# Kernel optimization log

Hardware: AMD Instinct MI355X
Metric: run time of the kernel (lower is better)

Reference implementation:

```python
import jax, jax.numpy as jnp
import numpy as np
import math

D_MODEL = 512
N_HEADS = 8
D_HEAD = D_MODEL // N_HEADS
TEMP = math.sqrt(D_HEAD)


def setup_inputs() -> dict:
    key = jax.random.key(0)
    k1, k2, k3, k4, k5, k6 = jax.random.split(key, 6)
    B, L = 4, 2048
    q = jax.random.normal(k1, (B, L, D_MODEL), dtype=jnp.float32)
    # bool mask, True -> zero out post-softmax attention (matches torch.where branch)
    mask = jax.random.bernoulli(k2, 0.1, (B, L, L))
    in_weight = jax.random.normal(k3, (3 * D_MODEL, D_MODEL), dtype=jnp.float32) * 0.02
    in_bias = jax.random.normal(k4, (3 * D_MODEL,), dtype=jnp.float32) * 0.02
    out_w = jax.random.normal(k5, (D_MODEL, D_MODEL), dtype=jnp.float32) * 0.02
    out_b = jax.random.normal(k6, (D_MODEL,), dtype=jnp.float32) * 0.02
    return {"q": q, "mask": mask, "in_weight": in_weight, "in_bias": in_bias,
            "out_w": out_w, "out_b": out_b}


def reference(q, mask, in_weight, in_bias, out_w, out_b):
    B, L, D = q.shape
    # per-head weight slicing exactly as the torch reshape: (H, E, 3, D)
    W = in_weight.reshape(N_HEADS, D_HEAD, 3, D)
    Bv = in_bias.reshape(N_HEADS, D_HEAD, 3)
    qw, kw, vw = W[:, :, 0, :], W[:, :, 1, :], W[:, :, 2, :]  # (H, E, D)
    qb, kb, vb = Bv[:, :, 0], Bv[:, :, 1], Bv[:, :, 2]        # (H, E)
    # self-attention: k = q, v = q (forward defaults)
    Q = jnp.einsum('bld,hed->bhle', q, qw) + qb[None, :, None, :]
    K = jnp.einsum('bld,hed->bhle', q, kw) + kb[None, :, None, :]
    V = jnp.einsum('bld,hed->bhle', q, vw) + vb[None, :, None, :]
    atn = jax.nn.softmax(jnp.einsum('bhqe,bhke->bhqk', Q, K) / TEMP, axis=-1)
    # post-softmax bool masking (faithful to the original non-standard order)
    atn = jnp.where(mask[:, None, :, :], jnp.zeros((), atn.dtype), atn)
    # QUIRK of source: attention() returns V (not atn @ V); heads = concat of V
    heads = V.transpose(0, 2, 1, 3).reshape(B, L, D)  # (B, L, D_MODEL)
    outputs = heads @ out_w.T + out_b
    masks = atn.sum(axis=1)  # sum over heads -> (B, Lq, Lk)
    return outputs, masks
```

## Files before the change

### kernel.cpp

```cpp
#include <hip/hip_runtime.h>

typedef unsigned short u16;
typedef unsigned int u32;
typedef __bf16 bf16x8 __attribute__((ext_vector_type(8)));
typedef float f32x4 __attribute__((ext_vector_type(4)));

#define B_SZ 4
#define L_SZ 2048
#define D_SZ 512
#define H_SZ 8
#define E_SZ 64

#define Q_SCALE 0.18033688011112042f

#define WS_FLAG   0
#define WS_WPACK  1024
#define WS_BPACK  (WS_WPACK + 1572864)
#define WS_WOUT   (WS_BPACK + 6144)
#define WS_QBF    (WS_WOUT + 524288)
#define WS_Q      (WS_QBF + 8388608)
#define WS_K      (WS_Q + 8388608)
#define WS_V      (WS_K + 8388608)
#define WS_STATS  (WS_V + 8388608)

static __device__ __forceinline__ u16 f2bf(float f) {
  unsigned int u = __float_as_uint(f);
  u += 0x7FFFu + ((u >> 16) & 1u);
  return (u16)(u >> 16);
}

static __device__ __forceinline__ float fexp2(float x) {
  return __builtin_amdgcn_exp2f(x);
}

union FragU { bf16x8 v; uint4 u4; unsigned long long ul[2]; };

static __device__ __forceinline__ int gperm(int d) {
  int t = d & 31;
  return (d & ~31) | ((t & 12) << 1) | ((t & 16) >> 2) | (t & 3);
}

static __device__ __forceinline__ bf16x8 qfrag(const u16* __restrict__ Qp,
                                               int row, int half, int lg) {
  FragU f;
  f.u4 = *reinterpret_cast<const uint4*>(
      (const char*)Qp + (size_t)row * 128 + (half << 6) + (lg << 4));
  return f.v;
}

static __device__ __forceinline__ void gload_lds16(const void* g, void* l) {
  __builtin_amdgcn_global_load_lds(
      (const __attribute__((address_space(1))) void*)g,
      (__attribute__((address_space(3))) void*)l, 16, 0, 0);
}

template<int NT, int NCHUNK>
static __device__ __forceinline__ void stage_ktile(const u16* __restrict__ Kh, int kb0,
                                                   char* tile, int tid) {
  int wbase = (tid & ~63) * 16;
#pragma unroll
  for (int i = 0; i < NCHUNK / NT; i++) {
    int cl = tid + i * NT;
    int r = cl >> 3, c = cl & 7;
    const char* g = (const char*)Kh + (size_t)(kb0 + r) * 128 + ((c ^ (r & 7)) << 4);
    gload_lds16(g, tile + wbase + i * NT * 16);
  }
}

static __device__ __forceinline__ bf16x8 lds_frag(const char* tile, int c, int half,
                                                  int lr, int lg) {
  int r = c * 16 + lr;
  int off = ((half << 6) | (lg << 4)) ^ ((r & 7) << 4);
  FragU f;
  f.u4 = *reinterpret_cast<const uint4*>(tile + r * 128 + off);
  return f.v;
}

__global__ __launch_bounds__(256) void kdetect(const unsigned int* __restrict__ w,
                                               int* __restrict__ flag) {
  int fB = 0, fF = 0;
  for (int i = blockIdx.x * blockDim.x + threadIdx.x; i < 262144;
       i += gridDim.x * blockDim.x) {
    unsigned int v = w[i];
    if (v == 0x3F800000u) fF = 1;
    else if (v > 1u) fB = 1;
  }
  if (__any(fB)) { if ((threadIdx.x & 63) == 0) atomicOr(&flag[0], 1); }
  if (__any(fF)) { if ((threadIdx.x & 63) == 0) atomicOr(&flag[1], 1); }
}

__global__ __launch_bounds__(256) void kcast(const float* __restrict__ q,
                                             u16* __restrict__ qbf) {
  int i = blockIdx.x * blockDim.x + threadIdx.x;
  int row = i >> 6, c = i & 63;
  int g = c >> 2, lg = c & 3;
  const float* src = q + (size_t)row * 512 + g * 32 + lg * 4;
  float4 v0 = *reinterpret_cast<const float4*>(src);
  float4 v1 = *reinterpret_cast<const float4*>(src + 16);
  u32 w0 = f2bf(v0.x) | ((u32)f2bf(v0.y) << 16);
  u32 w1 = f2bf(v0.z) | ((u32)f2bf(v0.w) << 16);
  u32 w2 = f2bf(v1.x) | ((u32)f2bf(v1.y) << 16);
  u32 w3 = f2bf(v1.z) | ((u32)f2bf(v1.w) << 16);
  uint4 out = {w0, w1, w2, w3};
  *reinterpret_cast<uint4*>(qbf + (size_t)row * 512 + c * 8) = out;
}

__global__ __launch_bounds__(256) void kpack(const float* __restrict__ w_in,
                                             const float* __restrict__ b_in,
                                             const float* __restrict__ w_out,
                                             u16* __restrict__ Wpack, float* __restrict__ bpack,
                                             u16* __restrict__ Wout) {
  const int T0 = 1536 * 512;
  const int T1 = T0 + 512 * 512;
  const int T2 = T1 + 1536;
  for (int i = blockIdx.x * blockDim.x + threadIdx.x; i < T2; i += gridDim.x * blockDim.x) {
    if (i < T0) {
      int n = i >> 9, d = i & 511;
      int sel = n >> 9, idx = n & 511;
      int h = idx >> 6, e = idx & 63;
      int row = h * 192 + e * 3 + sel;
      float v = w_in[row * 512 + d];
      if (sel == 0) v *= Q_SCALE;
      Wpack[(size_t)n * 512 + gperm(d)] = f2bf(v);
    } else if (i < T1) {
      int j = i - T0;
      int n = j >> 9, d = j & 511;
      Wout[(size_t)n * 512 + gperm(d)] = f2bf(w_out[j]);
    } else {
      int n = i - T1;
      int sel = n >> 9, idx = n & 511;
      int h = idx >> 6, e = idx & 63;
      int row = h * 192 + e * 3 + sel;
      float v = b_in[row];
      if (sel == 0) v *= Q_SCALE;
      bpack[n] = v;
    }
  }
}

static __device__ __forceinline__ void stage_tile(const u16* __restrict__ A,
                                                  const u16* __restrict__ Bw,
                                                  int m0, int n0, int t,
                                                  char* tA, char* tB, int tid) {
  int w64 = tid & ~63;
#pragma unroll
  for (int i = 0; i < 4; i++) {
    int cl = tid + i * 256;
    int r = cl >> 3, c = cl & 7;
    size_t gofs = (size_t)r * 1024 + t * 128 + ((c ^ (r & 7)) << 4);
    gload_lds16((const char*)A + (size_t)m0 * 1024 + gofs, tA + (i * 256 + w64) * 16);
    gload_lds16((const char*)Bw + (size_t)n0 * 1024 + gofs, tB + (i * 256 + w64) * 16);
  }
}

template<int MODE>
__global__ __launch_bounds__(256) void kgemm(const u16* __restrict__ A,
                                             const u16* __restrict__ Bw,
                                             const float* __restrict__ bias,
                                             u16* __restrict__ Qb, u16* __restrict__ Kb,
                                             u16* __restrict__ Vb, float* __restrict__ outp) {
  __shared__ __align__(128) char tA[2][16384], tB[2][16384];
  int tid = threadIdx.x;
  int w = tid >> 6, lane = tid & 63;
  int lr = lane & 15, lg = lane >> 4;
  int m0 = blockIdx.x * 128, n0 = blockIdx.y * 128;
  int wr = w >> 1, wc = w & 1;

  f32x4 acc[4][4] = {};

  stage_tile(A, Bw, m0, n0, 0, tA[0], tB[0], tid);
  __syncthreads();
#pragma unroll 1
  for (int t = 0; t < 8; t++) {
    if (t < 7) stage_tile(A, Bw, m0, n0, t + 1, tA[(t + 1) & 1], tB[(t + 1) & 1], tid);
    const char* mA = tA[t & 1] + wr * 64 * 128;
    const char* mB = tB[t & 1] + wc * 64 * 128;
#pragma unroll
    for (int gg = 0; gg < 2; gg++) {
      bf16x8 af[4], bf_[4];
#pragma unroll
      for (int i = 0; i < 4; i++) af[i] = lds_frag(mA, i, gg, lr, lg);
#pragma unroll
      for (int j = 0; j < 4; j++) bf_[j] = lds_frag(mB, j, gg, lr, lg);
#pragma unroll
      for (int i = 0; i < 4; i++)
#pragma unroll
        for (int j = 0; j < 4; j++)
          acc[i][j] = __builtin_amdgcn_mfma_f32_16x16x32_bf16(af[i], bf_[j], acc[i][j], 0, 0, 0);
    }
    __syncthreads();
  }

#pragma unroll
  for (int j = 0; j < 4; j++) {
    int col = n0 + wc * 64 + j * 16 + lr;
    float bb = bias[col];
#pragma unroll
    for (int i = 0; i < 4; i++) {
#pragma unroll
      for (int jj = 0; jj < 4; jj++) {
        int row = m0 + wr * 64 + i * 16 + lg * 4 + jj;
        float val = acc[i][j][jj] + bb;
        if (MODE == 1) {
          outp[(size_t)row * 512 + col] = val;
        } else {
          u16 bv = f2bf(val);
          int b = row >> 11, l = row & 2047;
          if (col < 512) {
            int h = col >> 6, e = col & 63;
            Qb[((((size_t)(b * 8 + h)) << 11) + l) * 64 + gperm(e)] = bv;
          } else if (col < 1024) {
            int c2 = col - 512, h = c2 >> 6, e = c2 & 63;
            Kb[((((size_t)(b * 8 + h)) << 11) + l) * 64 + gperm(e)] = bv;
          } else {
            Vb[(size_t)row * 512 + gperm(col - 1024)] = bv;
          }
        }
      }
    }
  }
}

__global__ __launch_bounds__(256, 4) void kstats(const u16* __restrict__ Qb,
                                                 const u16* __restrict__ Kb,
                                                 float* __restrict__ stats) {
  __shared__ __align__(128) char tile[2][8192];
  int bh = blockIdx.x;
  int tid = threadIdx.x;
  int w = tid >> 6, lane = tid & 63;
  int lr = lane & 15, lg = lane >> 4;
  int q0 = blockIdx.y * 64 + w * 16;
  const u16* Qp = Qb + (size_t)bh * L_SZ * E_SZ;
  const u16* Kp = Kb + (size_t)bh * L_SZ * E_SZ;

  bf16x8 bq0 = qfrag(Qp, q0 + lr, 0, lg);
  bf16x8 bq1 = qfrag(Qp, q0 + lr, 1, lg);
  float s0 = 0.0f;

  stage_ktile<256, 512>(Kp, 0, tile[0], tid);
  __syncthreads();
#pragma unroll 1
  for (int t = 0; t < 32; t++) {
    if (t + 1 < 32) stage_ktile<256, 512>(Kp, (t + 1) * 64, tile[(t + 1) & 1], tid);
    const char* tl = tile[t & 1];
#pragma unroll
    for (int c = 0; c < 4; c++) {
      bf16x8 a0 = lds_frag(tl, c, 0, lr, lg);
      bf16x8 a1 = lds_frag(tl, c, 1, lr, lg);
      f32x4 d = {0.f, 0.f, 0.f, 0.f};
      d = __builtin_amdgcn_mfma_f32_16x16x32_bf16(a0, bq0, d, 0, 0, 0);
      d = __builtin_amdgcn_mfma_f32_16x16x32_bf16(a1, bq1, d, 0, 0, 0);
      s0 += fexp2(d[0]) + fexp2(d[1]) + fexp2(d[2]) + fexp2(d[3]);
    }
    __syncthreads();
  }
  s0 += __shfl_xor(s0, 16);
  s0 += __shfl_xor(s0, 32);
  if (lane < 16) stats[(size_t)bh * L_SZ + q0 + lr] = 1.0f / s0;
}

#define KM_PACKMASK(BITS, QOFS)                                                  \
  {                                                                              \
    size_t moff = mb + (size_t)(q0 + (QOFS) + lr) * L_SZ + kb0;                  \
    if (mode == 0) {                                                             \
      _Pragma("unroll")                                                          \
      for (int c = 0; c < 2; c++) {                                              \
        int4 mi = *reinterpret_cast<const int4*>((const int*)mask + moff + c * 16 + lg * 4); \
        BITS |= (mi.x ? 1u : 0u) << (c * 4);                                     \
        BITS |= (mi.y ? 1u : 0u) << (c * 4 + 1);                                 \
        BITS |= (mi.z ? 1u : 0u) << (c * 4 + 2);                                 \
        BITS |= (mi.w ? 1u : 0u) << (c * 4 + 3);                                 \
      }                                                                          \
    } else if (mode == 1) {                                                      \
      _Pragma("unroll")                                                          \
      for (int c = 0; c < 2; c++) {                                              \
        u32 mw = *reinterpret_cast<const u32*>((const unsigned char*)mask + moff + c * 16 + lg * 4); \
        BITS |= ((mw & 0x000000FFu) ? 1u : 0u) << (c * 4);                       \
        BITS |= ((mw & 0x0000FF00u) ? 1u : 0u) << (c * 4 + 1);                   \
        BITS |= ((mw & 0x00FF0000u) ? 1u : 0u) << (c * 4 + 2);                   \
        BITS |= ((mw & 0xFF000000u) ? 1u : 0u) << (c * 4 + 3);                   \
      }                                                                          \
    } else {                                                                     \
      _Pragma("unroll")                                                          \
      for (int c = 0; c < 2; c++) {                                              \
        float4 mf = *reinterpret_cast<const float4*>((const float*)mask + moff + c * 16 + lg * 4); \
        BITS |= ((mf.x != 0.f) ? 1u : 0u) << (c * 4);                            \
        BITS |= ((mf.y != 0.f) ? 1u : 0u) << (c * 4 + 1);                        \
        BITS |= ((mf.z != 0.f) ? 1u : 0u) << (c * 4 + 2);                        \
        BITS |= ((mf.w != 0.f) ? 1u : 0u) << (c * 4 + 3);                        \
      }                                                                          \
    }                                                                            \
  }

__global__ __launch_bounds__(256, 4) void kmasks(const u16* __restrict__ Qb,
                                                 const u16* __restrict__ Kb,
                                                 const float* __restrict__ stats,
                                                 const void* __restrict__ mask,
                                                 const int* __restrict__ flag,
                                                 float* __restrict__ outp) {
  __shared__ __align__(128) char tile[32768];
  int b = blockIdx.z;
  int tid = threadIdx.x;
  int lane = tid & 63;
  int lr = lane & 15, lg = lane >> 4;
  int w = tid >> 6;
  int q0 = blockIdx.y * 64 + w * 16;
  int kb0 = blockIdx.x * 32;
  int mode = flag[0] ? 1 : (flag[1] ? 2 : 0);
  const size_t LE = (size_t)L_SZ * E_SZ;
  size_t mb = (size_t)b * L_SZ * L_SZ;

  {
    int wbase = (tid & ~63) * 16;
#pragma unroll
    for (int i = 0; i < 8; i++) {
      int r = tid >> 3, cc = tid & 7;
      const char* g = (const char*)(Kb + (size_t)(b * 8 + i) * LE)
                    + (size_t)(kb0 + r) * 128 + ((cc ^ (r & 7)) << 4);
      gload_lds16(g, tile + (i * 256 + (tid & ~63)) * 16 + (wbase - (tid & ~63) * 16));
    }
  }

  bf16x8 qh0[8], qh1[8];
  float rr[8];
#pragma unroll
  for (int h = 0; h < 8; h++) {
    const u16* Qp = Qb + (size_t)(b * 8 + h) * LE;
    qh0[h] = qfrag(Qp, q0 + lr, 0, lg);
    qh1[h] = qfrag(Qp, q0 + lr, 1, lg);
    rr[h] = stats[(size_t)(b * 8 + h) * L_SZ + q0 + lr];
  }

  u32 bits0 = 0;
  KM_PACKMASK(bits0, 0)

  __syncthreads();

  f32x4 P0 = {0.f, 0.f, 0.f, 0.f}, P1 = {0.f, 0.f, 0.f, 0.f};
#pragma unroll
  for (int h = 0; h < 8; h++) {
    const char* th = tile + h * 4096;
    {
      bf16x8 a0 = lds_frag(th, 0, 0, lr, lg);
      bf16x8 a1 = lds_frag(th, 0, 1, lr, lg);
      f32x4 d = {0.f, 0.f, 0.f, 0.f};
      d = __builtin_amdgcn_mfma_f32_16x16x32_bf16(a0, qh0[h], d, 0, 0, 0);
      d = __builtin_amdgcn_mfma_f32_16x16x32_bf16(a1, qh1[h], d, 0, 0, 0);
#pragma unroll
      for (int j = 0; j < 4; j++) P0[j] += fexp2(d[j]) * rr[h];
    }
    {
      bf16x8 a0 = lds_frag(th, 1, 0, lr, lg);
      bf16x8 a1 = lds_frag(th, 1, 1, lr, lg);
      f32x4 d = {0.f, 0.f, 0.f, 0.f};
      d = __builtin_amdgcn_mfma_f32_16x16x32_bf16(a0, qh0[h], d, 0, 0, 0);
      d = __builtin_amdgcn_mfma_f32_16x16x32_bf16(a1, qh1[h], d, 0, 0, 0);
#pragma unroll
      for (int j = 0; j < 4; j++) P1[j] += fexp2(d[j]) * rr[h];
    }
  }

  float* mrow = outp + (size_t)B_SZ * L_SZ * D_SZ + mb
              + (size_t)(q0 + lr) * L_SZ + kb0;
  {
    f32x4 v = P0;
    if ((bits0 >> 0) & 1u) v[0] = 0.f;
    if ((bits0 >> 1) & 1u) v[1] = 0.f;
    if ((bits0 >> 2) & 1u) v[2] = 0.f;
    if ((bits0 >> 3) & 1u) v[3] = 0.f;
    *reinterpret_cast<f32x4*>(mrow + lg * 4) = v;
  }
  {
    f32x4 v = P1;
    if ((bits0 >> 4) & 1u) v[0] = 0.f;
    if ((bits0 >> 5) & 1u) v[1] = 0.f;
    if ((bits0 >> 6) & 1u) v[2] = 0.f;
    if ((bits0 >> 7) & 1u) v[3] = 0.f;
    *reinterpret_cast<f32x4*>(mrow + 16 + lg * 4) = v;
  }
}

extern "C" void kernel_launch(void* const* d_in, const int* in_sizes, int n_in,
                              void* d_out, int out_size, void* d_ws, size_t ws_size,
                              hipStream_t stream) {
  (void)in_sizes; (void)n_in; (void)out_size; (void)ws_size;
  const float* q     = (const float*)d_in[0];
  const void*  mask  = d_in[1];
  const float* w_in  = (const float*)d_in[2];
  const float* b_in  = (const float*)d_in[3];
  const float* w_out = (const float*)d_in[4];
  const float* b_out = (const float*)d_in[5];
  float* outp = (float*)d_out;
  char* ws = (char*)d_ws;

  int*    flag  = (int*)(ws + WS_FLAG);
  u16*    Wpack = (u16*)(ws + WS_WPACK);
  float*  bpack = (float*)(ws + WS_BPACK);
  u16*    Wout  = (u16*)(ws + WS_WOUT);
  u16*    qbf   = (u16*)(ws + WS_QBF);
  u16*    Qb    = (u16*)(ws + WS_Q);
  u16*    Kb    = (u16*)(ws + WS_K);
  u16*    Vb    = (u16*)(ws + WS_V);
  float*  stats = (float*)(ws + WS_STATS);

  hipMemsetAsync(flag, 0, 16, stream);
  hipLaunchKernelGGL(kdetect, dim3(256), dim3(256), 0, stream, (const unsigned int*)mask, flag);
  hipLaunchKernelGGL(kcast, dim3(2048), dim3(256), 0, stream, q, qbf);
  hipLaunchKernelGGL(kpack, dim3(2048), dim3(256), 0, stream, w_in, b_in, w_out,
                     Wpack, bpack, Wout);
  hipLaunchKernelGGL((kgemm<0>), dim3(64, 12), dim3(256), 0, stream,
                     qbf, Wpack, bpack, Qb, Kb, Vb, (float*)nullptr);
  hipLaunchKernelGGL((kgemm<1>), dim3(64, 4), dim3(256), 0, stream,
                     Vb, Wout, b_out, (u16*)nullptr, (u16*)nullptr, (u16*)nullptr, outp);
  hipLaunchKernelGGL(kstats, dim3(32, 32), dim3(256), 0, stream, Qb, Kb, stats);
  hipLaunchKernelGGL(kmasks, dim3(64, 32, 4), dim3(256), 0, stream, Qb, Kb, stats, mask, flag, outp);
}
```

Measured before the change: 168.0 us.

## Enlarge kmasks tiles to reuse staged K across more query rows

The mask kernel now uses 512-thread blocks that stage a 64-key K tile for all 8 heads (64KB of LDS) once, then loop over 512 query rows in four 128-row chunks. Before, each block staged a 32-key tile and handled only 64 query rows. The goal is to cut redundant global K traffic and LDS staging per output element. In exchange, Q fragments and stats are now reloaded per head inside the loop, and the grid shrinks to 512 blocks with large LDS use, which lowers occupancy and latency hiding.

```diff
diff --git a/kernel.cpp b/kernel.cpp
--- a/kernel.cpp
+++ b/kernel.cpp
@@ -259,53 +259,20 @@
   if (lane < 16) stats[(size_t)bh * L_SZ + q0 + lr] = 1.0f / s0;
 }
 
-#define KM_PACKMASK(BITS, QOFS)                                                  \
-  {                                                                              \
-    size_t moff = mb + (size_t)(q0 + (QOFS) + lr) * L_SZ + kb0;                  \
-    if (mode == 0) {                                                             \
-      _Pragma("unroll")                                                          \
-      for (int c = 0; c < 2; c++) {                                              \
-        int4 mi = *reinterpret_cast<const int4*>((const int*)mask + moff + c * 16 + lg * 4); \
-        BITS |= (mi.x ? 1u : 0u) << (c * 4);                                     \
-        BITS |= (mi.y ? 1u : 0u) << (c * 4 + 1);                                 \
-        BITS |= (mi.z ? 1u : 0u) << (c * 4 + 2);                                 \
-        BITS |= (mi.w ? 1u : 0u) << (c * 4 + 3);                                 \
-      }                                                                          \
-    } else if (mode == 1) {                                                      \
-      _Pragma("unroll")                                                          \
-      for (int c = 0; c < 2; c++) {                                              \
-        u32 mw = *reinterpret_cast<const u32*>((const unsigned char*)mask + moff + c * 16 + lg * 4); \
-        BITS |= ((mw & 0x000000FFu) ? 1u : 0u) << (c * 4);                       \
-        BITS |= ((mw & 0x0000FF00u) ? 1u : 0u) << (c * 4 + 1);                   \
-        BITS |= ((mw & 0x00FF0000u) ? 1u : 0u) << (c * 4 + 2);                   \
-        BITS |= ((mw & 0xFF000000u) ? 1u : 0u) << (c * 4 + 3);                   \
-      }                                                                          \
-    } else {                                                                     \
-      _Pragma("unroll")                                                          \
-      for (int c = 0; c < 2; c++) {                                              \
-        float4 mf = *reinterpret_cast<const float4*>((const float*)mask + moff + c * 16 + lg * 4); \
-        BITS |= ((mf.x != 0.f) ? 1u : 0u) << (c * 4);                            \
-        BITS |= ((mf.y != 0.f) ? 1u : 0u) << (c * 4 + 1);                        \
-        BITS |= ((mf.z != 0.f) ? 1u : 0u) << (c * 4 + 2);                        \
-        BITS |= ((mf.w != 0.f) ? 1u : 0u) << (c * 4 + 3);                        \
-      }                                                                          \
-    }                                                                            \
-  }
-
-__global__ __launch_bounds__(256, 4) void kmasks(const u16* __restrict__ Qb,
+__global__ __launch_bounds__(512, 4) void kmasks(const u16* __restrict__ Qb,
                                                  const u16* __restrict__ Kb,
                                                  const float* __restrict__ stats,
                                                  const void* __restrict__ mask,
                                                  const int* __restrict__ flag,
                                                  float* __restrict__ outp) {
-  __shared__ __align__(128) char tile[32768];
+  __shared__ __align__(128) char tile[65536];
   int b = blockIdx.z;
   int tid = threadIdx.x;
   int lane = tid & 63;
   int lr = lane & 15, lg = lane >> 4;
   int w = tid >> 6;
-  int q0 = blockIdx.y * 64 + w * 16;
-  int kb0 = blockIdx.x * 32;
+  int kb0 = blockIdx.x * 64;
+  int qc0 = blockIdx.y * 512;
   int mode = flag[0] ? 1 : (flag[1] ? 2 : 0);
   const size_t LE = (size_t)L_SZ * E_SZ;
   size_t mb = (size_t)b * L_SZ * L_SZ;
@@ -314,69 +281,131 @@
     int wbase = (tid & ~63) * 16;
 #pragma unroll
     for (int i = 0; i < 8; i++) {
-      int r = tid >> 3, cc = tid & 7;
-      const char* g = (const char*)(Kb + (size_t)(b * 8 + i) * LE)
-                    + (size_t)(kb0 + r) * 128 + ((cc ^ (r & 7)) << 4);
-      gload_lds16(g, tile + (i * 256 + (tid & ~63)) * 16 + (wbase - (tid & ~63) * 16));
-    }
-  }
-
-  bf16x8 qh0[8], qh1[8];
-  float rr[8];
-#pragma unroll
-  for (int h = 0; h < 8; h++) {
-    const u16* Qp = Qb + (size_t)(b * 8 + h) * LE;
-    qh0[h] = qfrag(Qp, q0 + lr, 0, lg);
-    qh1[h] = qfrag(Qp, q0 + lr, 1, lg);
-    rr[h] = stats[(size_t)(b * 8 + h) * L_SZ + q0 + lr];
-  }
-
-  u32 bits0 = 0;
-  KM_PACKMASK(bits0, 0)
-
+      int cl = tid + i * 512;
+      int h = cl >> 9, cw = cl & 511;
+      int r = cw >> 3, c = cw & 7;
+      const char* g = (const char*)(Kb + (size_t)(b * 8 + h) * LE)
+                    + (size_t)(kb0 + r) * 128 + ((c ^ (r & 7)) << 4);
+      gload_lds16(g, tile + wbase + i * 512 * 16);
+    }
+  }
   __syncthreads();
 
-  f32x4 P0 = {0.f, 0.f, 0.f, 0.f}, P1 = {0.f, 0.f, 0.f, 0.f};
-#pragma unroll
-  for (int h = 0; h < 8; h++) {
-    const char* th = tile + h * 4096;
+#pragma unroll 1
+  for (int qi = 0; qi < 4; qi++) {
+    int q0 = qc0 + qi * 128 + w * 16;
+    size_t rowoff = mb + (size_t)(q0 + lr) * L_SZ + kb0;
+
+    u32 bits = 0;
+    if (mode == 0) {
+#pragma unroll
+      for (int c = 0; c < 4; c++) {
+        int4 mi = *reinterpret_cast<const int4*>((const int*)mask + rowoff + c * 16 + lg * 4);
+        bits |= (mi.x ? 1u : 0u) << (c * 4);
+        bits |= (mi.y ? 1u : 0u) << (c * 4 + 1);
+        bits |= (mi.z ? 1u : 0u) << (c * 4 + 2);
+        bits |= (mi.w ? 1u : 0u) << (c * 4 + 3);
+      }
+    } else if (mode == 1) {
+#pragma unroll
+      for (int c = 0; c < 4; c++) {
+        u32 mw = *reinterpret_cast<const u32*>((const unsigned char*)mask + rowoff + c * 16 + lg * 4);
+        bits |= ((mw & 0x000000FFu) ? 1u : 0u) << (c * 4);
+        bits |= ((mw & 0x0000FF00u) ? 1u : 0u) << (c * 4 + 1);
+        bits |= ((mw & 0x00FF0000u) ? 1u : 0u) << (c * 4 + 2);
+        bits |= ((mw & 0xFF000000u) ? 1u : 0u) << (c * 4 + 3);
+      }
+    } else {
+#pragma unroll
+      for (int c = 0; c < 4; c++) {
+        float4 mf = *reinterpret_cast<const float4*>((const float*)mask + rowoff + c * 16 + lg * 4);
+        bits |= ((mf.x != 0.f) ? 1u : 0u) << (c * 4);
+        bits |= ((mf.y != 0.f) ? 1u : 0u) << (c * 4 + 1);
+        bits |= ((mf.z != 0.f) ? 1u : 0u) << (c * 4 + 2);
+        bits |= ((mf.w != 0.f) ? 1u : 0u) << (c * 4 + 3);
+      }
+    }
+
+    f32x4 P0 = {0.f, 0.f, 0.f, 0.f}, P1 = {0.f, 0.f, 0.f, 0.f};
+    f32x4 P2 = {0.f, 0.f, 0.f, 0.f}, P3 = {0.f, 0.f, 0.f, 0.f};
+#pragma unroll
+    for (int h = 0; h < 8; h++) {
+      const u16* Qp = Qb + (size_t)(b * 8 + h) * LE;
+      bf16x8 bq0 = qfrag(Qp, q0 + lr, 0, lg);
+      bf16x8 bq1 = qfrag(Qp, q0 + lr, 1, lg);
+      float rr = stats[(size_t)(b * 8 + h) * L_SZ + q0 + lr];
+      const char* th = tile + h * 8192;
+      {
+        bf16x8 a0 = lds_frag(th, 0, 0, lr, lg);
+        bf16x8 a1 = lds_frag(th, 0, 1, lr, lg);
+        f32x4 d = {0.f, 0.f, 0.f, 0.f};
+        d = __builtin_amdgcn_mfma_f32_16x16x32_bf16(a0, bq0, d, 0, 0, 0);
+        d = __builtin_amdgcn_mfma_f32_16x16x32_bf16(a1, bq1, d, 0, 0, 0);
+#pragma unroll
+        for (int j = 0; j < 4; j++) P0[j] += fexp2(d[j]) * rr;
+      }
+      {
+        bf16x8 a0 = lds_frag(th, 1, 0, lr, lg);
+        bf16x8 a1 = lds_frag(th, 1, 1, lr, lg);
+        f32x4 d = {0.f, 0.f, 0.f, 0.f};
+        d = __builtin_amdgcn_mfma_f32_16x16x32_bf16(a0, bq0, d, 0, 0, 0);
+        d = __builtin_amdgcn_mfma_f32_16x16x32_bf16(a1, bq1, d, 0, 0, 0);
+#pragma unroll
+        for (int j = 0; j < 4; j++) P1[j] += fexp2(d[j]) * rr;
+      }
+      {
+        bf16x8 a0 = lds_frag(th, 2, 0, lr, lg);
+        bf16x8 a1 = lds_frag(th, 2, 1, lr, lg);
+        f32x4 d = {0.f, 0.f, 0.f, 0.f};
+        d = __builtin_amdgcn_mfma_f32_16x16x32_bf16(a0, bq0, d, 0, 0, 0);
+        d = __builtin_amdgcn_mfma_f32_16x16x32_bf16(a1, bq1, d, 0, 0, 0);
+#pragma unroll
+        for (int j = 0; j < 4; j++) P2[j] += fexp2(d[j]) * rr;
+      }
+      {
+        bf16x8 a0 = lds_frag(th, 3, 0, lr, lg);
+        bf16x8 a1 = lds_frag(th, 3, 1, lr, lg);
+        f32x4 d = {0.f, 0.f, 0.f, 0.f};
+        d = __builtin_amdgcn_mfma_f32_16x16x32_bf16(a0, bq0, d, 0, 0, 0);
+        d = __builtin_amdgcn_mfma_f32_16x16x32_bf16(a1, bq1, d, 0, 0, 0);
+#pragma unroll
+        for (int j = 0; j < 4; j++) P3[j] += fexp2(d[j]) * rr;
+      }
+    }
+
+    float* mrow = outp + (size_t)B_SZ * L_SZ * D_SZ + rowoff;
     {
-      bf16x8 a0 = lds_frag(th, 0, 0, lr, lg);
-      bf16x8 a1 = lds_frag(th, 0, 1, lr, lg);
-      f32x4 d = {0.f, 0.f, 0.f, 0.f};
-      d = __builtin_amdgcn_mfma_f32_16x16x32_bf16(a0, qh0[h], d, 0, 0, 0);
-      d = __builtin_amdgcn_mfma_f32_16x16x32_bf16(a1, qh1[h], d, 0, 0, 0);
-#pragma unroll
-      for (int j = 0; j < 4; j++) P0[j] += fexp2(d[j]) * rr[h];
+      f32x4 v = P0;
+      if ((bits >> 0) & 1u) v[0] = 0.f;
+      if ((bits >> 1) & 1u) v[1] = 0.f;
+      if ((bits >> 2) & 1u) v[2] = 0.f;
+      if ((bits >> 3) & 1u) v[3] = 0.f;
+      *reinterpret_cast<f32x4*>(mrow + 0 * 16 + lg * 4) = v;
     }
     {
-      bf16x8 a0 = lds_frag(th, 1, 0, lr, lg);
-      bf16x8 a1 = lds_frag(th, 1, 1, lr, lg);
-      f32x4 d = {0.f, 0.f, 0.f, 0.f};
-      d = __builtin_amdgcn_mfma_f32_16x16x32_bf16(a0, qh0[h], d, 0, 0, 0);
-      d = __builtin_amdgcn_mfma_f32_16x16x32_bf16(a1, qh1[h], d, 0, 0, 0);
-#pragma unroll
-      for (int j = 0; j < 4; j++) P1[j] += fexp2(d[j]) * rr[h];
-    }
-  }
-
-  float* mrow = outp + (size_t)B_SZ * L_SZ * D_SZ + mb
-              + (size_t)(q0 + lr) * L_SZ + kb0;
-  {
-    f32x4 v = P0;
-    if ((bits0 >> 0) & 1u) v[0] = 0.f;
-    if ((bits0 >> 1) & 1u) v[1] = 0.f;
-    if ((bits0 >> 2) & 1u) v[2] = 0.f;
-    if ((bits0 >> 3) & 1u) v[3] = 0.f;
-    *reinterpret_cast<f32x4*>(mrow + lg * 4) = v;
-  }
-  {
-    f32x4 v = P1;
-    if ((bits0 >> 4) & 1u) v[0] = 0.f;
-    if ((bits0 >> 5) & 1u) v[1] = 0.f;
-    if ((bits0 >> 6) & 1u) v[2] = 0.f;
-    if ((bits0 >> 7) & 1u) v[3] = 0.f;
-    *reinterpret_cast<f32x4*>(mrow + 16 + lg * 4) = v;
+      f32x4 v = P1;
+      if ((bits >> 4) & 1u) v[0] = 0.f;
+      if ((bits >> 5) & 1u) v[1] = 0.f;
+      if ((bits >> 6) & 1u) v[2] = 0.f;
+      if ((bits >> 7) & 1u) v[3] = 0.f;
+      *reinterpret_cast<f32x4*>(mrow + 1 * 16 + lg * 4) = v;
+    }
+    {
+      f32x4 v = P2;
+      if ((bits >> 8) & 1u) v[0] = 0.f;
+      if ((bits >> 9) & 1u) v[1] = 0.f;
+      if ((bits >> 10) & 1u) v[2] = 0.f;
+      if ((bits >> 11) & 1u) v[3] = 0.f;
+      *reinterpret_cast<f32x4*>(mrow + 2 * 16 + lg * 4) = v;
+    }
+    {
+      f32x4 v = P3;
+      if ((bits >> 12) & 1u) v[0] = 0.f;
+      if ((bits >> 13) & 1u) v[1] = 0.f;
+      if ((bits >> 14) & 1u) v[2] = 0.f;
+      if ((bits >> 15) & 1u) v[3] = 0.f;
+      *reinterpret_cast<f32x4*>(mrow + 3 * 16 + lg * 4) = v;
+    }
   }
 }
 
@@ -413,5 +442,5 @@
   hipLaunchKernelGGL((kgemm<1>), dim3(64, 4), dim3(256), 0, stream,
                      Vb, Wout, b_out, (u16*)nullptr, (u16*)nullptr, (u16*)nullptr, outp);
   hipLaunchKernelGGL(kstats, dim3(32, 32), dim3(256), 0, stream, Qb, Kb, stats);
-  hipLaunchKernelGGL(kmasks, dim3(64, 32, 4), dim3(256), 0, stream, Qb, Kb, stats, mask, flag, outp);
-}
+  hipLaunchKernelGGL(kmasks, dim3(32, 4, 4), dim3(512), 0, stream, Qb, Kb, stats, mask, flag, outp);
+}
```

New measurement: 425.3 us. 2.53x slower.
